# Performance work log

Hardware: AMD Instinct MI355X
Metric: run time of the kernel (lower is better)

The kernel has to match this reference:

```python
import jax, jax.numpy as jnp
import numpy as np

B, T, C, H = 4, 2048, 1024, 16
D = C // H  # head_dim = 64

def setup_inputs() -> dict:
    key = jax.random.key(0)
    k1, k2, k3 = jax.random.split(key, 3)
    x = jax.random.normal(k1, (B, T, C), dtype=jnp.float32)
    # Linear weights stored as (out_features, in_features) like torch; we apply x @ W.T
    w_attn = jax.random.normal(k2, (3 * C, C), dtype=jnp.float32) * (1.0 / np.sqrt(C))
    w_proj = jax.random.normal(k3, (C, C), dtype=jnp.float32) * (1.0 / np.sqrt(C))
    return {"x": x, "w_attn": w_attn, "w_proj": w_proj}

def reference(x, w_attn, w_proj):
    Bv, Tv, Cv = x.shape
    qkv = jnp.einsum('btc,fc->btf', x, w_attn)  # [B,T,3C]
    q, k, v = jnp.split(qkv, 3, axis=-1)
    # [B,H,T,D]
    q = q.reshape(Bv, Tv, H, D).transpose(0, 2, 1, 3)
    k = k.reshape(Bv, Tv, H, D).transpose(0, 2, 1, 3)
    v = v.reshape(Bv, Tv, H, D).transpose(0, 2, 1, 3)
    scale = 1.0 / np.sqrt(D).astype(np.float32)
    att = jnp.einsum('bhqd,bhkd->bhqk', q, k) * scale
    causal = jnp.tril(jnp.ones((Tv, Tv), dtype=bool))
    att = jnp.where(causal, att, -jnp.inf)
    att = jax.nn.softmax(att, axis=-1)
    y = jnp.einsum('bhqk,bhkd->bhqd', att, v)
    y = y.transpose(0, 2, 1, 3).reshape(Bv, Tv, Cv)
    return jnp.einsum('btc,oc->bto', y, w_proj)
```

## Files before the change

### kernel.cpp

```cpp
#include <hip/hip_runtime.h>
#include <cstdint>
#include <cstddef>

typedef __attribute__((ext_vector_type(8))) short short8;
typedef __attribute__((ext_vector_type(4))) float f32x4;
typedef unsigned int u32;

#define MFMA_BF16(a, b, c) __builtin_amdgcn_mfma_f32_16x16x32_bf16((a), (b), (c), 0, 0, 0)

__device__ __forceinline__ void async16(const void* g, void* l) {
  __builtin_amdgcn_global_load_lds(
      (const __attribute__((address_space(1))) u32*)g,
      (__attribute__((address_space(3))) u32*)l, 16, 0, 0);
}

__device__ __forceinline__ short f2bf(float f) {
  u32 u = __builtin_bit_cast(u32, f);
  u += 0x7fffu + ((u >> 16) & 1u);
  return (short)(u >> 16);
}

__device__ __forceinline__ u32 pack_bf16_trunc(float lo, float hi) {
  return __builtin_amdgcn_perm(__builtin_bit_cast(u32, hi),
                               __builtin_bit_cast(u32, lo), 0x07060302u);
}

__global__ __launch_bounds__(256) void cast_all_kernel(
    const float* __restrict__ x, const float* __restrict__ wa,
    const float* __restrict__ wp, short* __restrict__ xb,
    short* __restrict__ wab, short* __restrict__ wpb) {
  const int i = blockIdx.x * blockDim.x + threadIdx.x;
  const float4* src;
  short4* dst;
  float sc = 1.0f;
  if (i < 2097152) {
    src = (const float4*)x + i;
    dst = (short4*)xb + i;
  } else if (i < 2883584) {
    const int j = i - 2097152;
    if (j < 262144) sc = 0.18033688011112042f;
    src = (const float4*)wa + j;
    dst = (short4*)wab + j;
  } else {
    const int j = i - 2883584;
    src = (const float4*)wp + j;
    dst = (short4*)wpb + j;
  }
  float4 v = *src;
  short4 r;
  r.x = f2bf(v.x * sc); r.y = f2bf(v.y * sc);
  r.z = f2bf(v.z * sc); r.w = f2bf(v.w * sc);
  *dst = r;
}

template <bool OUT_BF16>
__global__ __launch_bounds__(256) void gemm_bt_kernel(
    const short* __restrict__ A, const short* __restrict__ Bt,
    void* __restrict__ Cv, int M, int N, int K) {
  __shared__ __align__(16) short As[128 * 64];
  __shared__ __align__(16) short Bs[128 * 64];

  const int tid  = threadIdx.x;
  const int lane = tid & 63;
  const int wave = tid >> 6;
  const int quad = lane >> 4;
  const int l15  = lane & 15;

  const int id  = blockIdx.y * gridDim.x + blockIdx.x;
  const int xcd = id & 7;
  const int j   = id >> 3;
  const int by  = xcd * 8 + (j & 7);
  const int bx  = j >> 3;
  const int bm  = by * 128;
  const int bn  = bx * 128;

  const int wm = (wave >> 1) * 64;
  const int wn = (wave & 1) * 64;

  f32x4 acc[4][4];
#pragma unroll
  for (int i = 0; i < 4; ++i)
#pragma unroll
    for (int jj = 0; jj < 4; ++jj) acc[i][jj] = (f32x4){0.f, 0.f, 0.f, 0.f};

  int srow[4], scol[4];
#pragma unroll
  for (int it = 0; it < 4; ++it) {
    const int s = tid + it * 256;
    srow[it] = s >> 3;
    scol[it] = ((s & 7) ^ (srow[it] & 7)) * 8;
  }
  const int xk = l15 & 7;

  for (int k0 = 0; k0 < K; k0 += 64) {
    __syncthreads();
#pragma unroll
    for (int it = 0; it < 4; ++it) {
      const int s = tid + it * 256;
      async16(A  + (size_t)(bm + srow[it]) * K + k0 + scol[it], &As[s * 8]);
      async16(Bt + (size_t)(bn + srow[it]) * K + k0 + scol[it], &Bs[s * 8]);
    }
    __syncthreads();

    short8 af[4][2], bf[4][2];
#pragma unroll
    for (int mt = 0; mt < 4; ++mt) {
      const int ra = (wm + mt * 16 + l15) * 64;
      af[mt][0] = *(const short8*)&As[ra + ((quad) ^ xk) * 8];
      af[mt][1] = *(const short8*)&As[ra + ((4 + quad) ^ xk) * 8];
    }
#pragma unroll
    for (int nt = 0; nt < 4; ++nt) {
      const int rb = (wn + nt * 16 + l15) * 64;
      bf[nt][0] = *(const short8*)&Bs[rb + ((quad) ^ xk) * 8];
      bf[nt][1] = *(const short8*)&Bs[rb + ((4 + quad) ^ xk) * 8];
    }
#pragma unroll
    for (int kk = 0; kk < 2; ++kk)
#pragma unroll
      for (int mt = 0; mt < 4; ++mt)
#pragma unroll
        for (int nt = 0; nt < 4; ++nt)
          acc[mt][nt] = MFMA_BF16(af[mt][kk], bf[nt][kk], acc[mt][nt]);
  }

#pragma unroll
  for (int mt = 0; mt < 4; ++mt) {
    const int r0e = bm + wm + mt * 16 + quad * 4;
#pragma unroll
    for (int nt = 0; nt < 4; ++nt) {
      const int c = bn + wn + nt * 16 + l15;
#pragma unroll
      for (int reg = 0; reg < 4; ++reg) {
        float v = acc[mt][nt][reg];
        if (OUT_BF16)
          ((short*)Cv)[(size_t)(r0e + reg) * N + c] = f2bf(v);
        else
          ((float*)Cv)[(size_t)(r0e + reg) * N + c] = v;
      }
    }
  }
}

__global__ __launch_bounds__(256) void vtrans_kernel(
    const short* __restrict__ qkv, short* __restrict__ vt2) {
  __shared__ __align__(16) short Ts[64 * 80];
  const int kt = blockIdx.x;
  const int t0 = kt * 64;
  const int bh = blockIdx.y;
  const int b = bh >> 4, h = bh & 15;
  const int tid = threadIdx.x;
#pragma unroll
  for (int it = 0; it < 2; ++it) {
    const int ci = tid + it * 256;
    const int t = ci >> 3, cw = ci & 7;
    short8 v = *(const short8*)(qkv + (size_t)(b * 2048 + t0 + t) * 3072 +
                                2048 + h * 64 + cw * 8);
    *(short8*)&Ts[t * 80 + cw * 8] = v;
  }
  __syncthreads();
#pragma unroll
  for (int it = 0; it < 2; ++it) {
    const int ci = tid + it * 256;
    const int d = ci >> 3, c2 = ci & 7;
    short tmp[8];
#pragma unroll
    for (int j = 0; j < 8; ++j) tmp[j] = Ts[(c2 * 8 + j) * 80 + d];
    short* dst = vt2 +
        (size_t)((bh * 32 + kt) * 8 + (d >> 4) * 2 + (c2 >> 2)) * 512 +
        ((c2 & 3) * 16 + (d & 15)) * 8;
    *(short8*)dst = *(short8*)tmp;
  }
}

__global__ __launch_bounds__(256, 4) void attn_kernel(
    const short* __restrict__ qkv, const short* __restrict__ vt2,
    short* __restrict__ y) {
  __shared__ __align__(16) short Ks[2][4096];
  __shared__ __align__(16) short Ps[4][1024];

  const int bh    = blockIdx.x;
  const int pairi = blockIdx.y;
  const int b = bh >> 4, h = bh & 15;
  const int tid  = threadIdx.x;
  const int lane = tid & 63;
  const int wave = tid >> 6;
  const int quad = lane >> 4, l15 = lane & 15;
  const int base_row = b * 2048;
  short* Pw = &Ps[wave][0];

  const int s0 = tid, s1 = tid + 256;
  const int r0s = s0 >> 3, c0s = (s0 & 7) ^ (r0s & 7);
  const int r1s = s1 >> 3, c1s = (s1 & 7) ^ (r1s & 7);
  const short* kbase0 = qkv + (size_t)(base_row + r0s) * 3072 + 1024 + h * 64 + c0s * 8;
  const short* kbase1 = qkv + (size_t)(base_row + r1s) * 3072 + 1024 + h * 64 + c1s * 8;

  const short* v2base = vt2 + (size_t)bh * 32 * 4096 + (size_t)lane * 8;

  const int xk = l15 & 7;

  for (int half = 0; half < 2; ++half) {
    const int qi  = half ? (31 - pairi) : pairi;
    const int nkt = qi + 1;
    const int qg0 = qi * 64 + wave * 16;

    short8 qf[2];
    {
      const short* qp = qkv +
          (size_t)(base_row + qg0 + l15) * 3072 + h * 64 + quad * 8;
      qf[0] = *(const short8*)qp;
      qf[1] = *(const short8*)(qp + 32);
    }
    float l_r = 0.f;
    f32x4 o[4];
#pragma unroll
    for (int dt = 0; dt < 4; ++dt) o[dt] = (f32x4){0.f, 0.f, 0.f, 0.f};

    async16(kbase0, &Ks[0][s0 * 8]);
    async16(kbase1, &Ks[0][s1 * 8]);

    for (int kt = 0; kt < nkt; ++kt) {
      const int kvb = kt * 64;
      __syncthreads();

      if (kt + 1 < nkt) {
        const int nb = (kt + 1) & 1;
        const size_t koff = (size_t)(kvb + 64) * 3072;
        async16(kbase0 + koff, &Ks[nb][s0 * 8]);
        async16(kbase1 + koff, &Ks[nb][s1 * 8]);
      }
      const short* Kb = &Ks[kt & 1][0];

      const short* vp = v2base + (size_t)kt * 4096;
      short8 vf[4][2];
#pragma unroll
      for (int dt = 0; dt < 4; ++dt) {
        vf[dt][0] = *(const short8*)(vp + (dt * 2 + 0) * 512);
        vf[dt][1] = *(const short8*)(vp + (dt * 2 + 1) * 512);
      }

      short8 kf[4][2];
#pragma unroll
      for (int nt = 0; nt < 4; ++nt) {
        kf[nt][0] = *(const short8*)&Kb[(nt * 16 + l15) * 64 + ((quad) ^ xk) * 8];
        kf[nt][1] = *(const short8*)&Kb[(nt * 16 + l15) * 64 + ((4 + quad) ^ xk) * 8];
      }

      f32x4 s[4];
#pragma unroll
      for (int nt = 0; nt < 4; ++nt) {
        s[nt] = MFMA_BF16(kf[nt][0], qf[0], ((f32x4){0.f, 0.f, 0.f, 0.f}));
        s[nt] = MFMA_BF16(kf[nt][1], qf[1], s[nt]);
      }

      float p[4][4];
      if (kvb + 64 <= qg0) {
#pragma unroll
        for (int nt = 0; nt < 4; ++nt)
#pragma unroll
          for (int r = 0; r < 4; ++r)
            p[nt][r] = __builtin_amdgcn_exp2f(s[nt][r]);
      } else {
        const int qrel = qg0 + l15 - kvb;
#pragma unroll
        for (int nt = 0; nt < 4; ++nt)
#pragma unroll
          for (int r = 0; r < 4; ++r) {
            const int kvl = nt * 16 + quad * 4 + r;
            p[nt][r] = (kvl <= qrel) ? __builtin_amdgcn_exp2f(s[nt][r]) : 0.f;
          }
      }

      float rs = ((p[0][0] + p[0][1]) + (p[0][2] + p[0][3])) +
                 ((p[1][0] + p[1][1]) + (p[1][2] + p[1][3])) +
                 ((p[2][0] + p[2][1]) + (p[2][2] + p[2][3])) +
                 ((p[3][0] + p[3][1]) + (p[3][2] + p[3][3]));
      rs += __shfl_xor(rs, 16);
      rs += __shfl_xor(rs, 32);
      l_r += rs;

#pragma unroll
      for (int nt = 0; nt < 4; ++nt) {
        u32 w0 = pack_bf16_trunc(p[nt][0], p[nt][1]);
        u32 w1 = pack_bf16_trunc(p[nt][2], p[nt][3]);
        const int p0 = 8 * nt + 2 * quad;
        u32* dst = (u32*)Pw + (p0 >> 4) * 256 + ((p0 >> 2) & 3) * 64 +
                   l15 * 4 + (p0 & 3);
        *(uint2*)dst = make_uint2(w0, w1);
      }
      short8 pf0 = *(const short8*)&Pw[quad * 128 + l15 * 8];
      short8 pf1 = *(const short8*)&Pw[512 + quad * 128 + l15 * 8];

#pragma unroll
      for (int dt = 0; dt < 4; ++dt) {
        o[dt] = MFMA_BF16(vf[dt][0], pf0, o[dt]);
        o[dt] = MFMA_BF16(vf[dt][1], pf1, o[dt]);
      }
    }

    {
      const float inv = 1.f / l_r;
#pragma unroll
      for (int dt = 0; dt < 4; ++dt) {
        const int d = dt * 16 + quad * 4;
        u32 w0 = pack_bf16_trunc(o[dt][0] * inv, o[dt][1] * inv);
        u32 w1 = pack_bf16_trunc(o[dt][2] * inv, o[dt][3] * inv);
        *(uint2*)&Pw[(d >> 5) * 512 + l15 * 32 + (d & 31)] = make_uint2(w0, w1);
      }
      const int qq = lane >> 2, ck = lane & 3;
      const size_t yrow = (size_t)(base_row + qg0 + qq);
#pragma unroll
      for (int kkd = 0; kkd < 2; ++kkd) {
        short8 vv = *(const short8*)&Pw[kkd * 512 + qq * 32 + ck * 8];
        *(short8*)(y + yrow * 1024 + h * 64 + kkd * 32 + ck * 8) = vv;
      }
    }
    __syncthreads();
  }
}

extern "C" void kernel_launch(void* const* d_in, const int* in_sizes, int n_in,
                              void* d_out, int out_size, void* d_ws,
                              size_t ws_size, hipStream_t stream) {
  const float* x  = (const float*)d_in[0];
  const float* wa = (const float*)d_in[1];
  const float* wp = (const float*)d_in[2];
  float* out = (float*)d_out;

  char* ws = (char*)d_ws;
  short* xb  = (short*)(ws + 0);
  short* wab = (short*)(ws + 16777216);
  short* wpb = (short*)(ws + 23068672);
  short* qkv = (short*)(ws + 25165824);
  short* yb  = (short*)(ws + 75497472);
  short* vtb = xb;

  cast_all_kernel<<<12288, 256, 0, stream>>>(x, wa, wp, xb, wab, wpb);

  gemm_bt_kernel<true><<<dim3(3072 / 128, 8192 / 128), 256, 0, stream>>>(
      xb, wab, (void*)qkv, 8192, 3072, 1024);

  vtrans_kernel<<<dim3(32, 64), 256, 0, stream>>>(qkv, vtb);

  attn_kernel<<<dim3(64, 16), 256, 0, stream>>>(qkv, vtb, yb);

  gemm_bt_kernel<false><<<dim3(1024 / 128, 8192 / 128), 256, 0, stream>>>(
      yb, wpb, (void*)out, 8192, 1024, 1024);
}
```

Before: 242.2 us.

## Stage 128-row K tiles per barrier and defer row-sum shuffle reduction

Doubles the K tile staged into LDS per iteration to 128 rows, processing two 64-row subtiles per barrier. This halves the number of __syncthreads and async-load rounds. The per-tile cross-lane row-sum shuffles move to the end, summing a per-lane partial. It also wraps MFMA groups in s_setprio to favour matrix issue. The cost is doubled K LDS, which may reduce occupancy, and a wasted half-tile load when only one subtile is needed.

```diff
diff --git a/kernel.cpp b/kernel.cpp
--- a/kernel.cpp
+++ b/kernel.cpp
@@ -176,7 +176,7 @@
 __global__ __launch_bounds__(256, 4) void attn_kernel(
     const short* __restrict__ qkv, const short* __restrict__ vt2,
     short* __restrict__ y) {
-  __shared__ __align__(16) short Ks[2][4096];
+  __shared__ __align__(16) short Ks[2][8192];
   __shared__ __align__(16) short Ps[4][1024];
 
   const int bh    = blockIdx.x;
@@ -189,20 +189,24 @@
   const int base_row = b * 2048;
   short* Pw = &Ps[wave][0];
 
-  const int s0 = tid, s1 = tid + 256;
-  const int r0s = s0 >> 3, c0s = (s0 & 7) ^ (r0s & 7);
-  const int r1s = s1 >> 3, c1s = (s1 & 7) ^ (r1s & 7);
-  const short* kbase0 = qkv + (size_t)(base_row + r0s) * 3072 + 1024 + h * 64 + c0s * 8;
-  const short* kbase1 = qkv + (size_t)(base_row + r1s) * 3072 + 1024 + h * 64 + c1s * 8;
+  int srow[4], scol[4];
+  const short* kb[4];
+#pragma unroll
+  for (int it = 0; it < 4; ++it) {
+    const int s = tid + it * 256;
+    srow[it] = s >> 3;
+    scol[it] = ((s & 7) ^ (srow[it] & 7)) * 8;
+    kb[it] = qkv + (size_t)(base_row + srow[it]) * 3072 + 1024 + h * 64 + scol[it];
+  }
 
   const short* v2base = vt2 + (size_t)bh * 32 * 4096 + (size_t)lane * 8;
 
   const int xk = l15 & 7;
 
   for (int half = 0; half < 2; ++half) {
-    const int qi  = half ? (31 - pairi) : pairi;
-    const int nkt = qi + 1;
-    const int qg0 = qi * 64 + wave * 16;
+    const int qi    = half ? (31 - pairi) : pairi;
+    const int nkt   = (qi + 2) >> 1;
+    const int qg0   = qi * 64 + wave * 16;
 
     short8 qf[2];
     {
@@ -211,94 +215,106 @@
       qf[0] = *(const short8*)qp;
       qf[1] = *(const short8*)(qp + 32);
     }
-    float l_r = 0.f;
+    float l_part = 0.f;
     f32x4 o[4];
 #pragma unroll
     for (int dt = 0; dt < 4; ++dt) o[dt] = (f32x4){0.f, 0.f, 0.f, 0.f};
 
-    async16(kbase0, &Ks[0][s0 * 8]);
-    async16(kbase1, &Ks[0][s1 * 8]);
+#pragma unroll
+    for (int it = 0; it < 4; ++it)
+      async16(kb[it], &Ks[0][(tid + it * 256) * 8]);
 
     for (int kt = 0; kt < nkt; ++kt) {
-      const int kvb = kt * 64;
       __syncthreads();
 
       if (kt + 1 < nkt) {
-        const int nb = (kt + 1) & 1;
-        const size_t koff = (size_t)(kvb + 64) * 3072;
-        async16(kbase0 + koff, &Ks[nb][s0 * 8]);
-        async16(kbase1 + koff, &Ks[nb][s1 * 8]);
+        const size_t koff = (size_t)(kt + 1) * 128 * 3072;
+#pragma unroll
+        for (int it = 0; it < 4; ++it)
+          async16(kb[it] + koff, &Ks[(kt + 1) & 1][(tid + it * 256) * 8]);
       }
       const short* Kb = &Ks[kt & 1][0];
 
-      const short* vp = v2base + (size_t)kt * 4096;
-      short8 vf[4][2];
-#pragma unroll
-      for (int dt = 0; dt < 4; ++dt) {
-        vf[dt][0] = *(const short8*)(vp + (dt * 2 + 0) * 512);
-        vf[dt][1] = *(const short8*)(vp + (dt * 2 + 1) * 512);
-      }
-
-      short8 kf[4][2];
-#pragma unroll
-      for (int nt = 0; nt < 4; ++nt) {
-        kf[nt][0] = *(const short8*)&Kb[(nt * 16 + l15) * 64 + ((quad) ^ xk) * 8];
-        kf[nt][1] = *(const short8*)&Kb[(nt * 16 + l15) * 64 + ((4 + quad) ^ xk) * 8];
-      }
-
-      f32x4 s[4];
-#pragma unroll
-      for (int nt = 0; nt < 4; ++nt) {
-        s[nt] = MFMA_BF16(kf[nt][0], qf[0], ((f32x4){0.f, 0.f, 0.f, 0.f}));
-        s[nt] = MFMA_BF16(kf[nt][1], qf[1], s[nt]);
-      }
-
-      float p[4][4];
-      if (kvb + 64 <= qg0) {
-#pragma unroll
-        for (int nt = 0; nt < 4; ++nt)
-#pragma unroll
-          for (int r = 0; r < 4; ++r)
-            p[nt][r] = __builtin_amdgcn_exp2f(s[nt][r]);
-      } else {
-        const int qrel = qg0 + l15 - kvb;
-#pragma unroll
-        for (int nt = 0; nt < 4; ++nt)
-#pragma unroll
-          for (int r = 0; r < 4; ++r) {
-            const int kvl = nt * 16 + quad * 4 + r;
-            p[nt][r] = (kvl <= qrel) ? __builtin_amdgcn_exp2f(s[nt][r]) : 0.f;
-          }
-      }
-
-      float rs = ((p[0][0] + p[0][1]) + (p[0][2] + p[0][3])) +
-                 ((p[1][0] + p[1][1]) + (p[1][2] + p[1][3])) +
-                 ((p[2][0] + p[2][1]) + (p[2][2] + p[2][3])) +
-                 ((p[3][0] + p[3][1]) + (p[3][2] + p[3][3]));
-      rs += __shfl_xor(rs, 16);
-      rs += __shfl_xor(rs, 32);
-      l_r += rs;
-
-#pragma unroll
-      for (int nt = 0; nt < 4; ++nt) {
-        u32 w0 = pack_bf16_trunc(p[nt][0], p[nt][1]);
-        u32 w1 = pack_bf16_trunc(p[nt][2], p[nt][3]);
-        const int p0 = 8 * nt + 2 * quad;
-        u32* dst = (u32*)Pw + (p0 >> 4) * 256 + ((p0 >> 2) & 3) * 64 +
-                   l15 * 4 + (p0 & 3);
-        *(uint2*)dst = make_uint2(w0, w1);
-      }
-      short8 pf0 = *(const short8*)&Pw[quad * 128 + l15 * 8];
-      short8 pf1 = *(const short8*)&Pw[512 + quad * 128 + l15 * 8];
-
-#pragma unroll
-      for (int dt = 0; dt < 4; ++dt) {
-        o[dt] = MFMA_BF16(vf[dt][0], pf0, o[dt]);
-        o[dt] = MFMA_BF16(vf[dt][1], pf1, o[dt]);
+#pragma unroll
+      for (int sub = 0; sub < 2; ++sub) {
+        const int kvb = kt * 128 + sub * 64;
+        if (kvb > qg0 + 15) break;
+
+        const short* vp = v2base + (size_t)(2 * kt + sub) * 4096;
+        short8 vf[4][2];
+#pragma unroll
+        for (int dt = 0; dt < 4; ++dt) {
+          vf[dt][0] = *(const short8*)(vp + (dt * 2 + 0) * 512);
+          vf[dt][1] = *(const short8*)(vp + (dt * 2 + 1) * 512);
+        }
+
+        short8 kf[4][2];
+#pragma unroll
+        for (int nt = 0; nt < 4; ++nt) {
+          const int rk = (sub * 64 + nt * 16 + l15) * 64;
+          kf[nt][0] = *(const short8*)&Kb[rk + ((quad) ^ xk) * 8];
+          kf[nt][1] = *(const short8*)&Kb[rk + ((4 + quad) ^ xk) * 8];
+        }
+
+        f32x4 s[4];
+        __builtin_amdgcn_s_setprio(1);
+#pragma unroll
+        for (int nt = 0; nt < 4; ++nt) {
+          s[nt] = MFMA_BF16(kf[nt][0], qf[0], ((f32x4){0.f, 0.f, 0.f, 0.f}));
+          s[nt] = MFMA_BF16(kf[nt][1], qf[1], s[nt]);
+        }
+        __builtin_amdgcn_s_setprio(0);
+
+        float p[4][4];
+        if (kvb + 64 <= qg0) {
+#pragma unroll
+          for (int nt = 0; nt < 4; ++nt)
+#pragma unroll
+            for (int r = 0; r < 4; ++r)
+              p[nt][r] = __builtin_amdgcn_exp2f(s[nt][r]);
+        } else {
+          const int qrel = qg0 + l15 - kvb;
+#pragma unroll
+          for (int nt = 0; nt < 4; ++nt)
+#pragma unroll
+            for (int r = 0; r < 4; ++r) {
+              const int kvl = nt * 16 + quad * 4 + r;
+              p[nt][r] = (kvl <= qrel) ? __builtin_amdgcn_exp2f(s[nt][r]) : 0.f;
+            }
+        }
+
+        float rs = ((p[0][0] + p[0][1]) + (p[0][2] + p[0][3])) +
+                   ((p[1][0] + p[1][1]) + (p[1][2] + p[1][3])) +
+                   ((p[2][0] + p[2][1]) + (p[2][2] + p[2][3])) +
+                   ((p[3][0] + p[3][1]) + (p[3][2] + p[3][3]));
+        l_part += rs;
+
+#pragma unroll
+        for (int nt = 0; nt < 4; ++nt) {
+          u32 w0 = pack_bf16_trunc(p[nt][0], p[nt][1]);
+          u32 w1 = pack_bf16_trunc(p[nt][2], p[nt][3]);
+          const int p0 = 8 * nt + 2 * quad;
+          u32* dst = (u32*)Pw + (p0 >> 4) * 256 + ((p0 >> 2) & 3) * 64 +
+                     l15 * 4 + (p0 & 3);
+          *(uint2*)dst = make_uint2(w0, w1);
+        }
+        short8 pf0 = *(const short8*)&Pw[quad * 128 + l15 * 8];
+        short8 pf1 = *(const short8*)&Pw[512 + quad * 128 + l15 * 8];
+
+        __builtin_amdgcn_s_setprio(1);
+#pragma unroll
+        for (int dt = 0; dt < 4; ++dt) {
+          o[dt] = MFMA_BF16(vf[dt][0], pf0, o[dt]);
+          o[dt] = MFMA_BF16(vf[dt][1], pf1, o[dt]);
+        }
+        __builtin_amdgcn_s_setprio(0);
       }
     }
 
     {
+      float l_r = l_part;
+      l_r += __shfl_xor(l_r, 16);
+      l_r += __shfl_xor(l_r, 32);
       const float inv = 1.f / l_r;
 #pragma unroll
       for (int dt = 0; dt < 4; ++dt) {
```

Measured after the change: 256.9 us. 6.1% more time.

## Triple-buffer K tiles with explicit vmcnt waits and defer row-sum shuffles

Applied to the files above, without the earlier changes.

The attention kernel's K tile staging moves from double to triple buffering. It prefetches two tiles ahead and uses explicit s_waitcnt vmcnt plus a raw s_barrier in place of __syncthreads, so each wait covers only the tile about to be used. MFMA blocks are wrapped in s_setprio to favour matrix issue, and the cross-quad row-sum shuffles are moved out of the loop into the epilogue. This costs more LDS per block, which could lower occupancy, and the correctness of the manual vmcnt counting depends on the V register loads also being counted.

```diff
diff --git a/kernel.cpp b/kernel.cpp
--- a/kernel.cpp
+++ b/kernel.cpp
@@ -176,7 +176,7 @@
 __global__ __launch_bounds__(256, 4) void attn_kernel(
     const short* __restrict__ qkv, const short* __restrict__ vt2,
     short* __restrict__ y) {
-  __shared__ __align__(16) short Ks[2][4096];
+  __shared__ __align__(16) short Ks[3][4096];
   __shared__ __align__(16) short Ps[4][1024];
 
   const int bh    = blockIdx.x;
@@ -211,25 +211,29 @@
       qf[0] = *(const short8*)qp;
       qf[1] = *(const short8*)(qp + 32);
     }
-    float l_r = 0.f;
+    float l_part = 0.f;
     f32x4 o[4];
 #pragma unroll
     for (int dt = 0; dt < 4; ++dt) o[dt] = (f32x4){0.f, 0.f, 0.f, 0.f};
 
     async16(kbase0, &Ks[0][s0 * 8]);
     async16(kbase1, &Ks[0][s1 * 8]);
-
+    if (nkt > 1) {
+      async16(kbase0 + (size_t)64 * 3072, &Ks[1][s0 * 8]);
+      async16(kbase1 + (size_t)64 * 3072, &Ks[1][s1 * 8]);
+    }
+
+    int cb = 0;
     for (int kt = 0; kt < nkt; ++kt) {
       const int kvb = kt * 64;
-      __syncthreads();
 
       if (kt + 1 < nkt) {
-        const int nb = (kt + 1) & 1;
-        const size_t koff = (size_t)(kvb + 64) * 3072;
-        async16(kbase0 + koff, &Ks[nb][s0 * 8]);
-        async16(kbase1 + koff, &Ks[nb][s1 * 8]);
-      }
-      const short* Kb = &Ks[kt & 1][0];
+        asm volatile("s_waitcnt vmcnt(2)" ::: "memory");
+      } else {
+        asm volatile("s_waitcnt vmcnt(0)" ::: "memory");
+      }
+      __builtin_amdgcn_sched_barrier(0);
+      __builtin_amdgcn_s_barrier();
 
       const short* vp = v2base + (size_t)kt * 4096;
       short8 vf[4][2];
@@ -238,6 +242,15 @@
         vf[dt][0] = *(const short8*)(vp + (dt * 2 + 0) * 512);
         vf[dt][1] = *(const short8*)(vp + (dt * 2 + 1) * 512);
       }
+      __builtin_amdgcn_sched_barrier(0);
+
+      if (kt + 2 < nkt) {
+        int pb = cb + 2; if (pb >= 3) pb -= 3;
+        const size_t koff = (size_t)(kvb + 128) * 3072;
+        async16(kbase0 + koff, &Ks[pb][s0 * 8]);
+        async16(kbase1 + koff, &Ks[pb][s1 * 8]);
+      }
+      const short* Kb = &Ks[cb][0];
 
       short8 kf[4][2];
 #pragma unroll
@@ -247,11 +260,13 @@
       }
 
       f32x4 s[4];
+      __builtin_amdgcn_s_setprio(1);
 #pragma unroll
       for (int nt = 0; nt < 4; ++nt) {
         s[nt] = MFMA_BF16(kf[nt][0], qf[0], ((f32x4){0.f, 0.f, 0.f, 0.f}));
         s[nt] = MFMA_BF16(kf[nt][1], qf[1], s[nt]);
       }
+      __builtin_amdgcn_s_setprio(0);
 
       float p[4][4];
       if (kvb + 64 <= qg0) {
@@ -275,9 +290,7 @@
                  ((p[1][0] + p[1][1]) + (p[1][2] + p[1][3])) +
                  ((p[2][0] + p[2][1]) + (p[2][2] + p[2][3])) +
                  ((p[3][0] + p[3][1]) + (p[3][2] + p[3][3]));
-      rs += __shfl_xor(rs, 16);
-      rs += __shfl_xor(rs, 32);
-      l_r += rs;
+      l_part += rs;
 
 #pragma unroll
       for (int nt = 0; nt < 4; ++nt) {
@@ -291,14 +304,21 @@
       short8 pf0 = *(const short8*)&Pw[quad * 128 + l15 * 8];
       short8 pf1 = *(const short8*)&Pw[512 + quad * 128 + l15 * 8];
 
+      __builtin_amdgcn_s_setprio(1);
 #pragma unroll
       for (int dt = 0; dt < 4; ++dt) {
         o[dt] = MFMA_BF16(vf[dt][0], pf0, o[dt]);
         o[dt] = MFMA_BF16(vf[dt][1], pf1, o[dt]);
       }
+      __builtin_amdgcn_s_setprio(0);
+
+      cb = (cb == 2) ? 0 : cb + 1;
     }
 
     {
+      float l_r = l_part;
+      l_r += __shfl_xor(l_r, 16);
+      l_r += __shfl_xor(l_r, 32);
       const float inv = 1.f / l_r;
 #pragma unroll
       for (int dt = 0; dt < 4; ++dt) {
```

Result: slower. 250.0 us (+3.2%).

## Add 256x256-tile double-buffered GEMM kernel for the QKV projection

Applied to the files above, without the earlier changes.

Replaces the 128x128 single-buffered QKV GEMM with a dedicated 256x256-tile kernel using 512 threads, 8 waves each computing 128x64, and double-buffered async global-to-LDS loads that prefetch the next K tile while computing the current one. Larger tiles raise arithmetic intensity and cut global traffic, and the XCD-aware block swizzle improves L2 locality. The cost is 128KB of LDS per block and a large accumulator register footprint, which limits occupancy. The output is written with scalar bf16 stores, which may be less coalesced.

```diff
diff --git a/kernel.cpp b/kernel.cpp
--- a/kernel.cpp
+++ b/kernel.cpp
@@ -53,6 +53,107 @@
   *dst = r;
 }
 
+__global__ __launch_bounds__(512, 2) void gemm256_kernel(
+    const short* __restrict__ A, const short* __restrict__ Bt,
+    short* __restrict__ C) {
+  __shared__ __align__(16) short As[2][16384];
+  __shared__ __align__(16) short Bs[2][16384];
+
+  const int tid  = threadIdx.x;
+  const int lane = tid & 63;
+  const int wave = tid >> 6;
+  const int quad = lane >> 4;
+  const int l15  = lane & 15;
+
+  const int id = blockIdx.y * gridDim.x + blockIdx.x;
+  const int sw = (id & 7) * 48 + (id >> 3);
+  const int by = sw / 12;
+  const int bx = sw % 12;
+  const int bm = by * 256;
+  const int bn = bx * 256;
+  const int wm = (wave >> 2) * 128;
+  const int wn = (wave & 3) * 64;
+
+  f32x4 acc[8][4];
+#pragma unroll
+  for (int mt = 0; mt < 8; ++mt)
+#pragma unroll
+    for (int nt = 0; nt < 4; ++nt) acc[mt][nt] = (f32x4){0.f, 0.f, 0.f, 0.f};
+
+  const short* abase[4];
+  const short* bbase[4];
+  int sdst[4];
+#pragma unroll
+  for (int it = 0; it < 4; ++it) {
+    const int s = tid + it * 512;
+    const int row = s >> 3;
+    const int chunk = (s & 7) ^ (row & 7);
+    abase[it] = A  + (size_t)(bm + row) * 1024 + chunk * 8;
+    bbase[it] = Bt + (size_t)(bn + row) * 1024 + chunk * 8;
+    sdst[it] = s * 8;
+  }
+  const int xk = l15 & 7;
+
+#pragma unroll
+  for (int it = 0; it < 4; ++it) {
+    async16(abase[it], &As[0][sdst[it]]);
+    async16(bbase[it], &Bs[0][sdst[it]]);
+  }
+
+  for (int kt = 0; kt < 16; ++kt) {
+    __builtin_amdgcn_s_barrier();
+
+    if (kt < 15) {
+      const int ko = (kt + 1) * 64;
+      const int nb = (kt + 1) & 1;
+#pragma unroll
+      for (int it = 0; it < 4; ++it) {
+        async16(abase[it] + ko, &As[nb][sdst[it]]);
+        async16(bbase[it] + ko, &Bs[nb][sdst[it]]);
+      }
+      asm volatile("s_waitcnt vmcnt(8)" ::: "memory");
+    } else {
+      asm volatile("s_waitcnt vmcnt(0)" ::: "memory");
+    }
+    __builtin_amdgcn_sched_barrier(0);
+    __builtin_amdgcn_s_barrier();
+
+    const short* Ab = &As[kt & 1][0];
+    const short* Bb = &Bs[kt & 1][0];
+#pragma unroll
+    for (int kk = 0; kk < 2; ++kk) {
+      short8 af[8], bf[4];
+#pragma unroll
+      for (int mt = 0; mt < 8; ++mt)
+        af[mt] = *(const short8*)&Ab[(wm + mt * 16 + l15) * 64 +
+                                     ((kk * 4 + quad) ^ xk) * 8];
+#pragma unroll
+      for (int nt = 0; nt < 4; ++nt)
+        bf[nt] = *(const short8*)&Bb[(wn + nt * 16 + l15) * 64 +
+                                     ((kk * 4 + quad) ^ xk) * 8];
+      __builtin_amdgcn_s_setprio(1);
+#pragma unroll
+      for (int mt = 0; mt < 8; ++mt)
+#pragma unroll
+        for (int nt = 0; nt < 4; ++nt)
+          acc[mt][nt] = MFMA_BF16(af[mt], bf[nt], acc[mt][nt]);
+      __builtin_amdgcn_s_setprio(0);
+    }
+  }
+
+#pragma unroll
+  for (int mt = 0; mt < 8; ++mt) {
+    const int r0e = bm + wm + mt * 16 + quad * 4;
+#pragma unroll
+    for (int nt = 0; nt < 4; ++nt) {
+      const int c = bn + wn + nt * 16 + l15;
+#pragma unroll
+      for (int reg = 0; reg < 4; ++reg)
+        C[(size_t)(r0e + reg) * 3072 + c] = f2bf(acc[mt][nt][reg]);
+    }
+  }
+}
+
 template <bool OUT_BF16>
 __global__ __launch_bounds__(256) void gemm_bt_kernel(
     const short* __restrict__ A, const short* __restrict__ Bt,
@@ -337,8 +438,7 @@
 
   cast_all_kernel<<<12288, 256, 0, stream>>>(x, wa, wp, xb, wab, wpb);
 
-  gemm_bt_kernel<true><<<dim3(3072 / 128, 8192 / 128), 256, 0, stream>>>(
-      xb, wab, (void*)qkv, 8192, 3072, 1024);
+  gemm256_kernel<<<dim3(12, 32), 512, 0, stream>>>(xb, wab, qkv);
 
   vtrans_kernel<<<dim3(32, 64), 256, 0, stream>>>(qkv, vtb);
 
```

Result: slower. 250.2 us (+3.3%).
